# Performance work log

Hardware: AMD Instinct MI355X
Metric: run time of the kernel (lower is better)

The kernel has to match this reference:

```python
import jax, jax.numpy as jnp
import numpy as np

N_NODES = 100000
N_EDGES = 1600000
IN_C, HID_C, OUT_C = 128, 256, 47


def setup_inputs() -> dict:
    key = jax.random.key(0)
    ks = jax.random.split(key, 8)
    x = jax.random.normal(ks[0], (N_NODES, IN_C), dtype=jnp.float32)
    edge_index = jax.random.randint(ks[1], (2, N_EDGES), 0, N_NODES, dtype=jnp.int64)

    def glorot(k, fan_in, fan_out):
        s = 1.0 / np.sqrt(fan_in)
        return jax.random.uniform(k, (fan_in, fan_out), jnp.float32, -s, s)

    W1_l = glorot(ks[2], IN_C, HID_C)
    b1 = jnp.zeros((HID_C,), jnp.float32)
    W1_r = glorot(ks[3], IN_C, HID_C)
    W2_l = glorot(ks[4], HID_C, OUT_C)
    b2 = jnp.zeros((OUT_C,), jnp.float32)
    W2_r = glorot(ks[5], HID_C, OUT_C)
    return {"x": x, "edge_index": edge_index,
            "W1_l": W1_l, "b1": b1, "W1_r": W1_r,
            "W2_l": W2_l, "b2": b2, "W2_r": W2_r}


def _sage_conv(x, src, dst, W_l, b, W_r, num_nodes):
    # mean aggregation of source-node features onto destination nodes
    msg_sum = jax.ops.segment_sum(x[src], dst, num_segments=num_nodes)  # [N, C]
    cnt = jax.ops.segment_sum(jnp.ones((src.shape[0], 1), x.dtype), dst,
                              num_segments=num_nodes)                   # [N, 1]
    mean = msg_sum / jnp.maximum(cnt, 1.0)
    # out = lin_l(mean) + lin_r(x_root); lin_l carries the bias (PyG default)
    return mean @ W_l + b + x @ W_r


def reference(x, edge_index, W1_l, b1, W1_r, W2_l, b2, W2_r):
    num_nodes = x.shape[0]
    src, dst = edge_index[0], edge_index[1]
    h = _sage_conv(x, src, dst, W1_l, b1, W1_r, num_nodes)
    h = jax.nn.relu(h)  # dropout is identity in eval mode
    out = _sage_conv(h, src, dst, W2_l, b2, W2_r, num_nodes)
    return jax.nn.log_softmax(out, axis=-1)
```

## Files before the change

kernel.cpp:

```cpp
#include <hip/hip_runtime.h>
#include <hip/hip_bf16.h>

constexpr int IN_C  = 128;
constexpr int HID_C = 256;
constexpr int OUT_C = 47;
constexpr int CAP   = 64;

typedef __attribute__((ext_vector_type(8))) short bf16x8;
typedef __attribute__((ext_vector_type(4))) float f32x4;

static __device__ __forceinline__ unsigned short f2bf(float v) {
  __hip_bfloat16 hb = __float2bfloat16(v);
  return *(unsigned short*)&hb;
}
static __device__ __forceinline__ float bf2f(unsigned short u) {
  return __uint_as_float((unsigned)u << 16);
}
static __device__ __forceinline__ float lof(unsigned u) { return __uint_as_float(u << 16); }
static __device__ __forceinline__ float hif(unsigned u) { return __uint_as_float(u & 0xffff0000u); }

__global__ __launch_bounds__(256) void fill_bucket(const int* __restrict__ src,
                                                   const int* __restrict__ dst,
                                                   int* __restrict__ cursor,
                                                   int* __restrict__ csr,
                                                   int E, int lo, int hi) {
  int e = blockIdx.x * blockDim.x + threadIdx.x;
  const int stride = gridDim.x * blockDim.x;
  for (; e < E; e += stride) {
    const int d = __builtin_nontemporal_load(&dst[e]);
    if (d >= lo && d < hi) {
      const int s = __builtin_nontemporal_load(&src[e]);
      const int p = atomicAdd(&cursor[d], 1);
      if (p < CAP) csr[(size_t)d * CAP + p] = s;
    }
  }
}

__global__ void f32_to_bf16(const float* __restrict__ in, unsigned short* __restrict__ out, int n4) {
  int i = blockIdx.x * blockDim.x + threadIdx.x;
  if (i < n4) {
    float4 v = *(const float4*)&in[i * 4];
    ushort4 o;
    o.x = f2bf(v.x); o.y = f2bf(v.y); o.z = f2bf(v.z); o.w = f2bf(v.w);
    *(ushort4*)&out[i * 4] = o;
  }
}

__global__ void build_weights(const float* __restrict__ W1l, const float* __restrict__ W1r,
                              const float* __restrict__ W2l, const float* __restrict__ W2r,
                              unsigned short* __restrict__ W1T, unsigned short* __restrict__ W2T) {
  int idx = blockIdx.x * blockDim.x + threadIdx.x;
  if (idx < 256 * 256) {
    int j = idx >> 8, k = idx & 255;
    float v = (k < 128) ? W1l[k * 256 + j] : W1r[(k - 128) * 256 + j];
    W1T[idx] = f2bf(v);
  } else if (idx < 256 * 256 + 128 * 256) {
    int t = idx - 256 * 256;
    int j = t >> 8, k = t & 255;
    float v = 0.f;
    if (j < OUT_C)                      v = W2l[k * OUT_C + j];
    else if (j >= 64 && j < 64 + OUT_C) v = W2r[k * OUT_C + (j - 64)];
    W2T[t] = f2bf(v);
  }
}

__global__ __launch_bounds__(256) void agg1(const unsigned short* __restrict__ xb,
                                            const int* __restrict__ cursor,
                                            const int* __restrict__ csr,
                                            unsigned short* __restrict__ meanb, int N) {
  const int wid  = (blockIdx.x * blockDim.x + threadIdx.x) >> 6;
  const int lane = threadIdx.x & 63;
  if (wid >= N) return;
  const unsigned* xw = (const unsigned*)xb;
  const int degr = cursor[wid];
  const int deg  = min(degr, CAP);
  const int idx  = (lane < deg) ? csr[(size_t)wid * CAP + lane] : 0;
  float a0 = 0.f, a1 = 0.f, b0 = 0.f, b1 = 0.f;
  float c0 = 0.f, c1 = 0.f, d0 = 0.f, d1 = 0.f;
  int e = 0;
  for (; e + 8 <= deg; e += 8) {
    const unsigned* r0 = xw + (size_t)__builtin_amdgcn_readlane(idx, e + 0) * 64;
    const unsigned* r1 = xw + (size_t)__builtin_amdgcn_readlane(idx, e + 1) * 64;
    const unsigned* r2 = xw + (size_t)__builtin_amdgcn_readlane(idx, e + 2) * 64;
    const unsigned* r3 = xw + (size_t)__builtin_amdgcn_readlane(idx, e + 3) * 64;
    const unsigned* r4 = xw + (size_t)__builtin_amdgcn_readlane(idx, e + 4) * 64;
    const unsigned* r5 = xw + (size_t)__builtin_amdgcn_readlane(idx, e + 5) * 64;
    const unsigned* r6 = xw + (size_t)__builtin_amdgcn_readlane(idx, e + 6) * 64;
    const unsigned* r7 = xw + (size_t)__builtin_amdgcn_readlane(idx, e + 7) * 64;
    const unsigned u0 = r0[lane], u1 = r1[lane], u2 = r2[lane], u3 = r3[lane];
    const unsigned u4 = r4[lane], u5 = r5[lane], u6 = r6[lane], u7 = r7[lane];
    a0 += lof(u0); a1 += hif(u0); b0 += lof(u1); b1 += hif(u1);
    c0 += lof(u2); c1 += hif(u2); d0 += lof(u3); d1 += hif(u3);
    a0 += lof(u4); a1 += hif(u4); b0 += lof(u5); b1 += hif(u5);
    c0 += lof(u6); c1 += hif(u6); d0 += lof(u7); d1 += hif(u7);
  }
  for (; e + 4 <= deg; e += 4) {
    const unsigned* r0 = xw + (size_t)__builtin_amdgcn_readlane(idx, e + 0) * 64;
    const unsigned* r1 = xw + (size_t)__builtin_amdgcn_readlane(idx, e + 1) * 64;
    const unsigned* r2 = xw + (size_t)__builtin_amdgcn_readlane(idx, e + 2) * 64;
    const unsigned* r3 = xw + (size_t)__builtin_amdgcn_readlane(idx, e + 3) * 64;
    const unsigned u0 = r0[lane], u1 = r1[lane], u2 = r2[lane], u3 = r3[lane];
    a0 += lof(u0); a1 += hif(u0); b0 += lof(u1); b1 += hif(u1);
    c0 += lof(u2); c1 += hif(u2); d0 += lof(u3); d1 += hif(u3);
  }
  for (; e < deg; ++e) {
    const unsigned* r0 = xw + (size_t)__builtin_amdgcn_readlane(idx, e) * 64;
    const unsigned u0 = r0[lane];
    a0 += lof(u0); a1 += hif(u0);
  }
  const float r0s = (a0 + b0) + (c0 + d0);
  const float r1s = (a1 + b1) + (c1 + d1);
  const float inv = (degr > 0) ? 1.0f / (float)degr : 0.0f;
  const unsigned wlo = f2bf(r0s * inv), whi = f2bf(r1s * inv);
  ((unsigned*)meanb)[(size_t)wid * 64 + lane] = wlo | (whi << 16);
}

template<int MODE>
__global__ __launch_bounds__(256) void gemm_mfma(const unsigned short* __restrict__ A0,
                                                 const unsigned short* __restrict__ A1,
                                                 const unsigned short* __restrict__ BT,
                                                 const float* __restrict__ bias,
                                                 unsigned short* __restrict__ Out,
                                                 unsigned short* __restrict__ OutR,
                                                 int M) {
  __shared__ unsigned short Asl[128 * 64];
  __shared__ unsigned short Bsl[128 * 64];
  const int tid  = threadIdx.x;
  const int wid  = tid >> 6, lane = tid & 63;
  const int wm   = wid >> 1, wn = wid & 1;
  const int r0   = blockIdx.x * 128;
  const int c0   = blockIdx.y * 128;

  f32x4 acc[4][4];
  #pragma unroll
  for (int m = 0; m < 4; ++m)
    #pragma unroll
    for (int n = 0; n < 4; ++n)
      #pragma unroll
      for (int j = 0; j < 4; ++j) acc[m][n][j] = 0.f;

  const int srow = lane >> 3;
  const int cs   = (lane & 7) ^ srow;
  const int fr   = lane & 15;
  const int klo  = (lane >> 4) * 16;
  const int swz  = (fr & 7) << 4;

  #pragma unroll 1
  for (int kb = 0; kb < 4; ++kb) {
    const unsigned short* Ap;
    int acol, ak;
    if (MODE == 0) { Ap = (kb < 2) ? A0 : A1; acol = (kb & 1) * 64; ak = 128; }
    else           { Ap = A0;                 acol = kb * 64;       ak = 256; }
    #pragma unroll
    for (int i = 0; i < 4; ++i) {
      const int rl = wid * 32 + i * 8 + srow;
      int gr = r0 + rl; if (gr > M - 1) gr = M - 1;
      const unsigned short* gsa = Ap + (size_t)gr * ak + acol + cs * 8;
      __builtin_amdgcn_global_load_lds(
          (const __attribute__((address_space(1))) unsigned int*)gsa,
          (__attribute__((address_space(3))) unsigned int*)&Asl[(wid * 32 + i * 8) * 64],
          16, 0, 0);
      const unsigned short* gsb = BT + (size_t)(c0 + rl) * 256 + kb * 64 + cs * 8;
      __builtin_amdgcn_global_load_lds(
          (const __attribute__((address_space(1))) unsigned int*)gsb,
          (__attribute__((address_space(3))) unsigned int*)&Bsl[(wid * 32 + i * 8) * 64],
          16, 0, 0);
    }
    asm volatile("s_waitcnt vmcnt(0)");
    __syncthreads();
    #pragma unroll
    for (int ks = 0; ks < 2; ++ks) {
      bf16x8 af[4], bfv[4];
      #pragma unroll
      for (int m = 0; m < 4; ++m) {
        const int ro = (wm * 64 + m * 16 + fr) * 128 + ((ks * 64 + klo) ^ swz);
        af[m] = *(const bf16x8*)((const char*)Asl + ro);
      }
      #pragma unroll
      for (int n = 0; n < 4; ++n) {
        const int ro = (wn * 64 + n * 16 + fr) * 128 + ((ks * 64 + klo) ^ swz);
        bfv[n] = *(const bf16x8*)((const char*)Bsl + ro);
      }
      #pragma unroll
      for (int m = 0; m < 4; ++m)
        #pragma unroll
        for (int n = 0; n < 4; ++n)
          acc[m][n] = __builtin_amdgcn_mfma_f32_16x16x32_bf16(af[m], bfv[n], acc[m][n], 0, 0, 0);
    }
    __syncthreads();
  }

  const int orow0 = r0 + wm * 64 + (lane >> 4) * 4;
  const int ocol0 = c0 + wn * 64 + (lane & 15);
  #pragma unroll
  for (int m = 0; m < 4; ++m) {
    #pragma unroll
    for (int n = 0; n < 4; ++n) {
      const int col = ocol0 + n * 16;
      const float badd = (MODE == 0) ? bias[col] : 0.f;
      #pragma unroll
      for (int j = 0; j < 4; ++j) {
        const int row = orow0 + m * 16 + j;
        if (row < M) {
          float v = acc[m][n][j] + badd;
          if (MODE == 0) {
            v = fmaxf(v, 0.f);
            Out[(size_t)row * HID_C + col] = f2bf(v);
          } else {
            if (col < 64) Out[(size_t)row * 64 + col] = f2bf(v);
            else          OutR[(size_t)row * 64 + (col - 64)] = f2bf(v);
          }
        }
      }
    }
  }
}

__global__ __launch_bounds__(256) void final_kernel(const unsigned short* __restrict__ Ol,
                                                    const unsigned short* __restrict__ Or,
                                                    const int* __restrict__ cursor,
                                                    const int* __restrict__ csr,
                                                    const float* __restrict__ b2,
                                                    float* __restrict__ out, int N) {
  const int wid  = (blockIdx.x * blockDim.x + threadIdx.x) >> 6;
  const int lane = threadIdx.x & 63;
  if (wid >= N) return;
  const int degr = cursor[wid];
  const int deg  = min(degr, CAP);
  const int idx  = (lane < deg) ? csr[(size_t)wid * CAP + lane] : 0;
  const bool act = lane < OUT_C;
  const int cl = act ? lane : 0;
  float t0 = 0.f, t1 = 0.f, t2 = 0.f, t3 = 0.f;
  int e = 0;
  for (; e + 8 <= deg; e += 8) {
    const unsigned short* r0 = Ol + (size_t)__builtin_amdgcn_readlane(idx, e + 0) * 64;
    const unsigned short* r1 = Ol + (size_t)__builtin_amdgcn_readlane(idx, e + 1) * 64;
    const unsigned short* r2 = Ol + (size_t)__builtin_amdgcn_readlane(idx, e + 2) * 64;
    const unsigned short* r3 = Ol + (size_t)__builtin_amdgcn_readlane(idx, e + 3) * 64;
    const unsigned short* r4 = Ol + (size_t)__builtin_amdgcn_readlane(idx, e + 4) * 64;
    const unsigned short* r5 = Ol + (size_t)__builtin_amdgcn_readlane(idx, e + 5) * 64;
    const unsigned short* r6 = Ol + (size_t)__builtin_amdgcn_readlane(idx, e + 6) * 64;
    const unsigned short* r7 = Ol + (size_t)__builtin_amdgcn_readlane(idx, e + 7) * 64;
    t0 += bf2f(r0[lane]); t1 += bf2f(r1[lane]);
    t2 += bf2f(r2[lane]); t3 += bf2f(r3[lane]);
    t0 += bf2f(r4[lane]); t1 += bf2f(r5[lane]);
    t2 += bf2f(r6[lane]); t3 += bf2f(r7[lane]);
  }
  for (; e + 4 <= deg; e += 4) {
    const unsigned short* r0 = Ol + (size_t)__builtin_amdgcn_readlane(idx, e + 0) * 64;
    const unsigned short* r1 = Ol + (size_t)__builtin_amdgcn_readlane(idx, e + 1) * 64;
    const unsigned short* r2 = Ol + (size_t)__builtin_amdgcn_readlane(idx, e + 2) * 64;
    const unsigned short* r3 = Ol + (size_t)__builtin_amdgcn_readlane(idx, e + 3) * 64;
    t0 += bf2f(r0[lane]); t1 += bf2f(r1[lane]);
    t2 += bf2f(r2[lane]); t3 += bf2f(r3[lane]);
  }
  for (; e < deg; ++e) {
    const unsigned short* r0 = Ol + (size_t)__builtin_amdgcn_readlane(idx, e) * 64;
    t0 += bf2f(r0[lane]);
  }
  const float sum = (t0 + t1) + (t2 + t3);
  const float inv = (degr > 0) ? 1.0f / (float)degr : 0.0f;
  float v = sum * inv + b2[cl] + bf2f(Or[(size_t)wid * 64 + cl]);
  if (!act) v = -INFINITY;
  float m = v;
  #pragma unroll
  for (int o = 32; o > 0; o >>= 1) m = fmaxf(m, __shfl_xor(m, o, 64));
  float ex = act ? expf(v - m) : 0.f;
  float s = ex;
  #pragma unroll
  for (int o = 32; o > 0; o >>= 1) s += __shfl_xor(s, o, 64);
  if (act) out[(size_t)wid * OUT_C + lane] = v - m - logf(s);
}


extern "C" void kernel_launch(void* const* d_in, const int* in_sizes, int n_in,
                              void* d_out, int out_size, void* d_ws, size_t ws_size,
                              hipStream_t stream) {
  const float* x   = (const float*)d_in[0];
  const int*   ei  = (const int*)d_in[1];
  const float* W1l = (const float*)d_in[2];
  const float* b1  = (const float*)d_in[3];
  const float* W1r = (const float*)d_in[4];
  const float* W2l = (const float*)d_in[5];
  const float* b2  = (const float*)d_in[6];
  const float* W2r = (const float*)d_in[7];
  float* out = (float*)d_out;

  const int N = in_sizes[0] / IN_C;
  const int E = in_sizes[1] / 2;
  const int* src = ei;
  const int* dst = ei + E;

  char* base = (char*)d_ws;
  size_t o = 0;
  auto take = [&](size_t bytes) -> char* {
    char* p = base + o;
    o = (o + bytes + 255) & ~(size_t)255;
    return p;
  };
  int* cursor = (int*)take((size_t)N * 4);
  const size_t zero_bytes = o;
  int* csr    = (int*)take((size_t)N * CAP * 4);
  unsigned short* xb    = (unsigned short*)take((size_t)N * IN_C * 2);
  unsigned short* meanb = (unsigned short*)take((size_t)N * IN_C * 2);
  unsigned short* h     = (unsigned short*)take((size_t)N * HID_C * 2);
  unsigned short* W1T   = (unsigned short*)take((size_t)256 * 256 * 2);
  unsigned short* W2T   = (unsigned short*)take((size_t)128 * 256 * 2);
  unsigned short* Ol    = meanb;
  unsigned short* Or    = meanb + (size_t)N * 64;
  (void)ws_size; (void)n_in; (void)out_size;

  hipMemsetAsync(base, 0, zero_bytes, stream);

  const int tb = 256;

  const int P = 8;
  const int chunk = (N + P - 1) / P;
  for (int p = 0; p < P; ++p) {
    const int lo = p * chunk;
    const int hi = min(N, lo + chunk);
    fill_bucket<<<2048, tb, 0, stream>>>(src, dst, cursor, csr, E, lo, hi);
  }

  const int n4 = N * IN_C / 4;
  f32_to_bf16<<<(n4 + tb - 1) / tb, tb, 0, stream>>>(x, xb, n4);
  build_weights<<<384, 256, 0, stream>>>(W1l, W1r, W2l, W2r, W1T, W2T);

  agg1<<<(N + 3) / 4, 256, 0, stream>>>(xb, cursor, csr, meanb, N);

  const int mb = (N + 127) / 128;
  gemm_mfma<0><<<dim3(mb, 2), 256, 0, stream>>>(meanb, xb, W1T, b1, h, nullptr, N);
  gemm_mfma<1><<<dim3(mb, 1), 256, 0, stream>>>(h, nullptr, W2T, nullptr, Ol, Or, N);

  final_kernel<<<(N + 3) / 4, 256, 0, stream>>>(Ol, Or, cursor, csr, b2, out, N);
}
```

Before: 405.6 us.

## Gather FP8-quantized features in both neighbor aggregation kernels

The input features are also converted to packed FP8 (stored in the h buffer before it is overwritten), and agg1 gathers 2 bytes per lane instead of 4, halving the random-gather traffic for layer 1. The layer-2 GEMM now writes its lin_l projection as FP8 bytes, so final_kernel gathers 1 byte per lane instead of 2. Both changes cut memory bandwidth in the gather-bound aggregation stages. The cost is lower precision in the aggregated messages, which may hurt accuracy against the tolerance.

```diff
diff --git a/kernel.cpp b/kernel.cpp
--- a/kernel.cpp
+++ b/kernel.cpp
@@ -8,6 +8,7 @@
 
 typedef __attribute__((ext_vector_type(8))) short bf16x8;
 typedef __attribute__((ext_vector_type(4))) float f32x4;
+typedef __attribute__((ext_vector_type(2))) float f32x2;
 
 static __device__ __forceinline__ unsigned short f2bf(float v) {
   __hip_bfloat16 hb = __float2bfloat16(v);
@@ -16,8 +17,6 @@
 static __device__ __forceinline__ float bf2f(unsigned short u) {
   return __uint_as_float((unsigned)u << 16);
 }
-static __device__ __forceinline__ float lof(unsigned u) { return __uint_as_float(u << 16); }
-static __device__ __forceinline__ float hif(unsigned u) { return __uint_as_float(u & 0xffff0000u); }
 
 __global__ __launch_bounds__(256) void fill_bucket(const int* __restrict__ src,
                                                    const int* __restrict__ dst,
@@ -36,13 +35,18 @@
   }
 }
 
-__global__ void f32_to_bf16(const float* __restrict__ in, unsigned short* __restrict__ out, int n4) {
+__global__ void f32_convert(const float* __restrict__ in,
+                            unsigned short* __restrict__ outb,
+                            unsigned int* __restrict__ outq, int n4) {
   int i = blockIdx.x * blockDim.x + threadIdx.x;
   if (i < n4) {
     float4 v = *(const float4*)&in[i * 4];
     ushort4 o;
     o.x = f2bf(v.x); o.y = f2bf(v.y); o.z = f2bf(v.z); o.w = f2bf(v.w);
-    *(ushort4*)&out[i * 4] = o;
+    *(ushort4*)&outb[i * 4] = o;
+    int p = __builtin_amdgcn_cvt_pk_fp8_f32(v.x, v.y, 0, false);
+    p     = __builtin_amdgcn_cvt_pk_fp8_f32(v.z, v.w, p, true);
+    outq[i] = (unsigned)p;
   }
 }
 
@@ -64,14 +68,13 @@
   }
 }
 
-__global__ __launch_bounds__(256) void agg1(const unsigned short* __restrict__ xb,
+__global__ __launch_bounds__(256) void agg1(const unsigned short* __restrict__ xq,
                                             const int* __restrict__ cursor,
                                             const int* __restrict__ csr,
                                             unsigned short* __restrict__ meanb, int N) {
   const int wid  = (blockIdx.x * blockDim.x + threadIdx.x) >> 6;
   const int lane = threadIdx.x & 63;
   if (wid >= N) return;
-  const unsigned* xw = (const unsigned*)xb;
   const int degr = cursor[wid];
   const int deg  = min(degr, CAP);
   const int idx  = (lane < deg) ? csr[(size_t)wid * CAP + lane] : 0;
@@ -79,34 +82,40 @@
   float c0 = 0.f, c1 = 0.f, d0 = 0.f, d1 = 0.f;
   int e = 0;
   for (; e + 8 <= deg; e += 8) {
-    const unsigned* r0 = xw + (size_t)__builtin_amdgcn_readlane(idx, e + 0) * 64;
-    const unsigned* r1 = xw + (size_t)__builtin_amdgcn_readlane(idx, e + 1) * 64;
-    const unsigned* r2 = xw + (size_t)__builtin_amdgcn_readlane(idx, e + 2) * 64;
-    const unsigned* r3 = xw + (size_t)__builtin_amdgcn_readlane(idx, e + 3) * 64;
-    const unsigned* r4 = xw + (size_t)__builtin_amdgcn_readlane(idx, e + 4) * 64;
-    const unsigned* r5 = xw + (size_t)__builtin_amdgcn_readlane(idx, e + 5) * 64;
-    const unsigned* r6 = xw + (size_t)__builtin_amdgcn_readlane(idx, e + 6) * 64;
-    const unsigned* r7 = xw + (size_t)__builtin_amdgcn_readlane(idx, e + 7) * 64;
-    const unsigned u0 = r0[lane], u1 = r1[lane], u2 = r2[lane], u3 = r3[lane];
-    const unsigned u4 = r4[lane], u5 = r5[lane], u6 = r6[lane], u7 = r7[lane];
-    a0 += lof(u0); a1 += hif(u0); b0 += lof(u1); b1 += hif(u1);
-    c0 += lof(u2); c1 += hif(u2); d0 += lof(u3); d1 += hif(u3);
-    a0 += lof(u4); a1 += hif(u4); b0 += lof(u5); b1 += hif(u5);
-    c0 += lof(u6); c1 += hif(u6); d0 += lof(u7); d1 += hif(u7);
+    const unsigned short* r0 = xq + (size_t)__builtin_amdgcn_readlane(idx, e + 0) * 64;
+    const unsigned short* r1 = xq + (size_t)__builtin_amdgcn_readlane(idx, e + 1) * 64;
+    const unsigned short* r2 = xq + (size_t)__builtin_amdgcn_readlane(idx, e + 2) * 64;
+    const unsigned short* r3 = xq + (size_t)__builtin_amdgcn_readlane(idx, e + 3) * 64;
+    const unsigned short* r4 = xq + (size_t)__builtin_amdgcn_readlane(idx, e + 4) * 64;
+    const unsigned short* r5 = xq + (size_t)__builtin_amdgcn_readlane(idx, e + 5) * 64;
+    const unsigned short* r6 = xq + (size_t)__builtin_amdgcn_readlane(idx, e + 6) * 64;
+    const unsigned short* r7 = xq + (size_t)__builtin_amdgcn_readlane(idx, e + 7) * 64;
+    const unsigned short q0 = r0[lane], q1 = r1[lane], q2 = r2[lane], q3 = r3[lane];
+    const unsigned short q4 = r4[lane], q5 = r5[lane], q6 = r6[lane], q7 = r7[lane];
+    { f32x2 v = __builtin_amdgcn_cvt_pk_f32_fp8((int)q0, false); a0 += v[0]; a1 += v[1]; }
+    { f32x2 v = __builtin_amdgcn_cvt_pk_f32_fp8((int)q1, false); b0 += v[0]; b1 += v[1]; }
+    { f32x2 v = __builtin_amdgcn_cvt_pk_f32_fp8((int)q2, false); c0 += v[0]; c1 += v[1]; }
+    { f32x2 v = __builtin_amdgcn_cvt_pk_f32_fp8((int)q3, false); d0 += v[0]; d1 += v[1]; }
+    { f32x2 v = __builtin_amdgcn_cvt_pk_f32_fp8((int)q4, false); a0 += v[0]; a1 += v[1]; }
+    { f32x2 v = __builtin_amdgcn_cvt_pk_f32_fp8((int)q5, false); b0 += v[0]; b1 += v[1]; }
+    { f32x2 v = __builtin_amdgcn_cvt_pk_f32_fp8((int)q6, false); c0 += v[0]; c1 += v[1]; }
+    { f32x2 v = __builtin_amdgcn_cvt_pk_f32_fp8((int)q7, false); d0 += v[0]; d1 += v[1]; }
   }
   for (; e + 4 <= deg; e += 4) {
-    const unsigned* r0 = xw + (size_t)__builtin_amdgcn_readlane(idx, e + 0) * 64;
-    const unsigned* r1 = xw + (size_t)__builtin_amdgcn_readlane(idx, e + 1) * 64;
-    const unsigned* r2 = xw + (size_t)__builtin_amdgcn_readlane(idx, e + 2) * 64;
-    const unsigned* r3 = xw + (size_t)__builtin_amdgcn_readlane(idx, e + 3) * 64;
-    const unsigned u0 = r0[lane], u1 = r1[lane], u2 = r2[lane], u3 = r3[lane];
-    a0 += lof(u0); a1 += hif(u0); b0 += lof(u1); b1 += hif(u1);
-    c0 += lof(u2); c1 += hif(u2); d0 += lof(u3); d1 += hif(u3);
+    const unsigned short* r0 = xq + (size_t)__builtin_amdgcn_readlane(idx, e + 0) * 64;
+    const unsigned short* r1 = xq + (size_t)__builtin_amdgcn_readlane(idx, e + 1) * 64;
+    const unsigned short* r2 = xq + (size_t)__builtin_amdgcn_readlane(idx, e + 2) * 64;
+    const unsigned short* r3 = xq + (size_t)__builtin_amdgcn_readlane(idx, e + 3) * 64;
+    const unsigned short q0 = r0[lane], q1 = r1[lane], q2 = r2[lane], q3 = r3[lane];
+    { f32x2 v = __builtin_amdgcn_cvt_pk_f32_fp8((int)q0, false); a0 += v[0]; a1 += v[1]; }
+    { f32x2 v = __builtin_amdgcn_cvt_pk_f32_fp8((int)q1, false); b0 += v[0]; b1 += v[1]; }
+    { f32x2 v = __builtin_amdgcn_cvt_pk_f32_fp8((int)q2, false); c0 += v[0]; c1 += v[1]; }
+    { f32x2 v = __builtin_amdgcn_cvt_pk_f32_fp8((int)q3, false); d0 += v[0]; d1 += v[1]; }
   }
   for (; e < deg; ++e) {
-    const unsigned* r0 = xw + (size_t)__builtin_amdgcn_readlane(idx, e) * 64;
-    const unsigned u0 = r0[lane];
-    a0 += lof(u0); a1 += hif(u0);
+    const unsigned short* r0 = xq + (size_t)__builtin_amdgcn_readlane(idx, e) * 64;
+    const unsigned short q0 = r0[lane];
+    { f32x2 v = __builtin_amdgcn_cvt_pk_f32_fp8((int)q0, false); a0 += v[0]; a1 += v[1]; }
   }
   const float r0s = (a0 + b0) + (c0 + d0);
   const float r1s = (a1 + b1) + (c1 + d1);
@@ -121,6 +130,7 @@
                                                  const unsigned short* __restrict__ BT,
                                                  const float* __restrict__ bias,
                                                  unsigned short* __restrict__ Out,
+                                                 unsigned char* __restrict__ OutQ,
                                                  unsigned short* __restrict__ OutR,
                                                  int M) {
   __shared__ unsigned short Asl[128 * 64];
@@ -207,8 +217,12 @@
             v = fmaxf(v, 0.f);
             Out[(size_t)row * HID_C + col] = f2bf(v);
           } else {
-            if (col < 64) Out[(size_t)row * 64 + col] = f2bf(v);
-            else          OutR[(size_t)row * 64 + (col - 64)] = f2bf(v);
+            if (col < 64) {
+              const int pk = __builtin_amdgcn_cvt_pk_fp8_f32(v, 0.f, 0, false);
+              OutQ[(size_t)row * 64 + col] = (unsigned char)(pk & 0xff);
+            } else {
+              OutR[(size_t)row * 64 + (col - 64)] = f2bf(v);
+            }
           }
         }
       }
@@ -216,7 +230,7 @@
   }
 }
 
-__global__ __launch_bounds__(256) void final_kernel(const unsigned short* __restrict__ Ol,
+__global__ __launch_bounds__(256) void final_kernel(const unsigned char* __restrict__ Olq,
                                                     const unsigned short* __restrict__ Or,
                                                     const int* __restrict__ cursor,
                                                     const int* __restrict__ csr,
@@ -233,30 +247,39 @@
   float t0 = 0.f, t1 = 0.f, t2 = 0.f, t3 = 0.f;
   int e = 0;
   for (; e + 8 <= deg; e += 8) {
-    const unsigned short* r0 = Ol + (size_t)__builtin_amdgcn_readlane(idx, e + 0) * 64;
-    const unsigned short* r1 = Ol + (size_t)__builtin_amdgcn_readlane(idx, e + 1) * 64;
-    const unsigned short* r2 = Ol + (size_t)__builtin_amdgcn_readlane(idx, e + 2) * 64;
-    const unsigned short* r3 = Ol + (size_t)__builtin_amdgcn_readlane(idx, e + 3) * 64;
-    const unsigned short* r4 = Ol + (size_t)__builtin_amdgcn_readlane(idx, e + 4) * 64;
-    const unsigned short* r5 = Ol + (size_t)__builtin_amdgcn_readlane(idx, e + 5) * 64;
-    const unsigned short* r6 = Ol + (size_t)__builtin_amdgcn_readlane(idx, e + 6) * 64;
-    const unsigned short* r7 = Ol + (size_t)__builtin_amdgcn_readlane(idx, e + 7) * 64;
-    t0 += bf2f(r0[lane]); t1 += bf2f(r1[lane]);
-    t2 += bf2f(r2[lane]); t3 += bf2f(r3[lane]);
-    t0 += bf2f(r4[lane]); t1 += bf2f(r5[lane]);
-    t2 += bf2f(r6[lane]); t3 += bf2f(r7[lane]);
+    const unsigned char* r0 = Olq + (size_t)__builtin_amdgcn_readlane(idx, e + 0) * 64;
+    const unsigned char* r1 = Olq + (size_t)__builtin_amdgcn_readlane(idx, e + 1) * 64;
+    const unsigned char* r2 = Olq + (size_t)__builtin_amdgcn_readlane(idx, e + 2) * 64;
+    const unsigned char* r3 = Olq + (size_t)__builtin_amdgcn_readlane(idx, e + 3) * 64;
+    const unsigned char* r4 = Olq + (size_t)__builtin_amdgcn_readlane(idx, e + 4) * 64;
+    const unsigned char* r5 = Olq + (size_t)__builtin_amdgcn_readlane(idx, e + 5) * 64;
+    const unsigned char* r6 = Olq + (size_t)__builtin_amdgcn_readlane(idx, e + 6) * 64;
+    const unsigned char* r7 = Olq + (size_t)__builtin_amdgcn_readlane(idx, e + 7) * 64;
+    const unsigned q0 = r0[lane], q1 = r1[lane], q2 = r2[lane], q3 = r3[lane];
+    const unsigned q4 = r4[lane], q5 = r5[lane], q6 = r6[lane], q7 = r7[lane];
+    t0 += __builtin_amdgcn_cvt_pk_f32_fp8((int)q0, false)[0];
+    t1 += __builtin_amdgcn_cvt_pk_f32_fp8((int)q1, false)[0];
+    t2 += __builtin_amdgcn_cvt_pk_f32_fp8((int)q2, false)[0];
+    t3 += __builtin_amdgcn_cvt_pk_f32_fp8((int)q3, false)[0];
+    t0 += __builtin_amdgcn_cvt_pk_f32_fp8((int)q4, false)[0];
+    t1 += __builtin_amdgcn_cvt_pk_f32_fp8((int)q5, false)[0];
+    t2 += __builtin_amdgcn_cvt_pk_f32_fp8((int)q6, false)[0];
+    t3 += __builtin_amdgcn_cvt_pk_f32_fp8((int)q7, false)[0];
   }
   for (; e + 4 <= deg; e += 4) {
-    const unsigned short* r0 = Ol + (size_t)__builtin_amdgcn_readlane(idx, e + 0) * 64;
-    const unsigned short* r1 = Ol + (size_t)__builtin_amdgcn_readlane(idx, e + 1) * 64;
-    const unsigned short* r2 = Ol + (size_t)__builtin_amdgcn_readlane(idx, e + 2) * 64;
-    const unsigned short* r3 = Ol + (size_t)__builtin_amdgcn_readlane(idx, e + 3) * 64;
-    t0 += bf2f(r0[lane]); t1 += bf2f(r1[lane]);
-    t2 += bf2f(r2[lane]); t3 += bf2f(r3[lane]);
+    const unsigned char* r0 = Olq + (size_t)__builtin_amdgcn_readlane(idx, e + 0) * 64;
+    const unsigned char* r1 = Olq + (size_t)__builtin_amdgcn_readlane(idx, e + 1) * 64;
+    const unsigned char* r2 = Olq + (size_t)__builtin_amdgcn_readlane(idx, e + 2) * 64;
+    const unsigned char* r3 = Olq + (size_t)__builtin_amdgcn_readlane(idx, e + 3) * 64;
+    const unsigned q0 = r0[lane], q1 = r1[lane], q2 = r2[lane], q3 = r3[lane];
+    t0 += __builtin_amdgcn_cvt_pk_f32_fp8((int)q0, false)[0];
+    t1 += __builtin_amdgcn_cvt_pk_f32_fp8((int)q1, false)[0];
+    t2 += __builtin_amdgcn_cvt_pk_f32_fp8((int)q2, false)[0];
+    t3 += __builtin_amdgcn_cvt_pk_f32_fp8((int)q3, false)[0];
   }
   for (; e < deg; ++e) {
-    const unsigned short* r0 = Ol + (size_t)__builtin_amdgcn_readlane(idx, e) * 64;
-    t0 += bf2f(r0[lane]);
+    const unsigned char* r0 = Olq + (size_t)__builtin_amdgcn_readlane(idx, e) * 64;
+    t0 += __builtin_amdgcn_cvt_pk_f32_fp8((int)r0[lane], false)[0];
   }
   const float sum = (t0 + t1) + (t2 + t3);
   const float inv = (degr > 0) ? 1.0f / (float)degr : 0.0f;
@@ -306,8 +329,9 @@
   unsigned short* h     = (unsigned short*)take((size_t)N * HID_C * 2);
   unsigned short* W1T   = (unsigned short*)take((size_t)256 * 256 * 2);
   unsigned short* W2T   = (unsigned short*)take((size_t)128 * 256 * 2);
-  unsigned short* Ol    = meanb;
-  unsigned short* Or    = meanb + (size_t)N * 64;
+  unsigned short* xq    = h;
+  unsigned char*  Olq   = (unsigned char*)meanb;
+  unsigned short* Or    = (unsigned short*)((char*)meanb + (size_t)N * 64);
   (void)ws_size; (void)n_in; (void)out_size;
 
   hipMemsetAsync(base, 0, zero_bytes, stream);
@@ -323,14 +347,14 @@
   }
 
   const int n4 = N * IN_C / 4;
-  f32_to_bf16<<<(n4 + tb - 1) / tb, tb, 0, stream>>>(x, xb, n4);
+  f32_convert<<<(n4 + tb - 1) / tb, tb, 0, stream>>>(x, xb, (unsigned int*)xq, n4);
   build_weights<<<384, 256, 0, stream>>>(W1l, W1r, W2l, W2r, W1T, W2T);
 
-  agg1<<<(N + 3) / 4, 256, 0, stream>>>(xb, cursor, csr, meanb, N);
+  agg1<<<(N + 3) / 4, 256, 0, stream>>>(xq, cursor, csr, meanb, N);
 
   const int mb = (N + 127) / 128;
-  gemm_mfma<0><<<dim3(mb, 2), 256, 0, stream>>>(meanb, xb, W1T, b1, h, nullptr, N);
-  gemm_mfma<1><<<dim3(mb, 1), 256, 0, stream>>>(h, nullptr, W2T, nullptr, Ol, Or, N);
-
-  final_kernel<<<(N + 3) / 4, 256, 0, stream>>>(Ol, Or, cursor, csr, b2, out, N);
-}
+  gemm_mfma<0><<<dim3(mb, 2), 256, 0, stream>>>(meanb, xb, W1T, b1, h, nullptr, nullptr, N);
+  gemm_mfma<1><<<dim3(mb, 1), 256, 0, stream>>>(h, nullptr, W2T, nullptr, nullptr, Olq, Or, N);
+
+  final_kernel<<<(N + 3) / 4, 256, 0, stream>>>(Olq, Or, cursor, csr, b2, out, N);
+}
```

After: 396.0 us. -2.4%, faster.
